# Kernel optimization log

Hardware: AMD Instinct MI355X
Metric: run time of the kernel (lower is better)

Reference implementation:

```python
import jax, jax.numpy as jnp
import numpy as np


def hilbert_perm(M: int) -> np.ndarray:
    """Permutation ordering the first M cells of a Hilbert curve on a 2^k x 2^k grid."""
    side = 1
    while side * side < M:
        side *= 2
    idx = np.arange(M)
    x = (idx % side).astype(np.int64)
    y = (idx // side).astype(np.int64)
    d = np.zeros(M, dtype=np.int64)
    s = side // 2
    while s > 0:
        rx = ((x & s) > 0).astype(np.int64)
        ry = ((y & s) > 0).astype(np.int64)
        d += s * s * ((3 * rx) ^ ry)
        swap = ry == 0
        flip = swap & (rx == 1)
        x2 = np.where(flip, s - 1 - x, x)
        y2 = np.where(flip, s - 1 - y, y)
        x, y = np.where(swap, y2, x2), np.where(swap, x2, y2)
        s //= 2
    return np.argsort(d, kind='stable')


SEGMENT_SIZE = 512


def setup_inputs() -> dict:
    key = jax.random.key(0)
    ks = jax.random.split(key, 5)
    B, M, H, D = 2, 8192, 8, 64
    hd = H * D  # 512
    q = jax.random.normal(ks[0], (B, M, H, D), dtype=jnp.float32)
    k = jax.random.normal(ks[1], (B, M, H, D), dtype=jnp.float32)
    v = jax.random.normal(ks[2], (B, M, H, D), dtype=jnp.float32)
    w_qkv = jax.random.normal(ks[3], (3 * hd, hd), dtype=jnp.float32) * (hd ** -0.5)
    w_out = jax.random.normal(ks[4], (hd, hd), dtype=jnp.float32) * (hd ** -0.5)
    return {"q": q, "k": k, "v": v, "w_qkv": w_qkv, "w_out": w_out}


def reference(q, k, v, w_qkv, w_out):
    B, M, H, D = q.shape
    hd = H * D
    S = SEGMENT_SIZE
    n_seg = M // S
    # Wrapper: mean over heads, then channel-repeat to hidden_dim
    x = q.mean(axis=2)                       # [B, M, D]
    x = jnp.tile(x, (1, 1, H))               # [B, M, hd]
    # HilbertAttentionCore: fused QKV projection
    qkv = jnp.einsum('bmc,fc->bmf', x, w_qkv)  # [B, M, 3*hd]
    qh, kh, vh = jnp.split(qkv, 3, axis=-1)
    # Hilbert-curve reordering (static permutation of seq dim)
    perm = jnp.asarray(hilbert_perm(M))
    inv = jnp.argsort(perm)
    def seg(t):
        t = t[:, perm]                       # reorder seq
        return t.reshape(B, n_seg, S, H, D)
    qs, ks_, vs = seg(qh), seg(kh), seg(vh)
    scale = D ** -0.5
    scores = jnp.einsum('bnshd,bnthd->bnhst', qs, ks_) * scale  # [B,n_seg,H,S,S]
    attn = jax.nn.softmax(scores, axis=-1)
    out = jnp.einsum('bnhst,bnthd->bnshd', attn, vs)            # [B,n_seg,S,H,D]
    out = out.reshape(B, M, hd)[:, inv]      # undo Hilbert ordering
    out = jnp.einsum('bmc,fc->bmf', out, w_out)  # output projection
    return out.reshape(B, M, H, D)
```

## Files before the change

kernel.cpp:

```cpp
#include <hip/hip_runtime.h>


typedef short bfrag __attribute__((ext_vector_type(8)));
typedef float ffrag __attribute__((ext_vector_type(4)));
typedef short svec4 __attribute__((ext_vector_type(4)));
typedef unsigned uvec4 __attribute__((ext_vector_type(4)));

__device__ inline short f2bf(float x) {
  unsigned u = __builtin_bit_cast(unsigned, x);
  u = (u + 0x7fffu + ((u >> 16) & 1u)) >> 16;
  return (short)u;
}
__device__ inline unsigned pk2f(float a, float b) {
  unsigned ua = (__builtin_bit_cast(unsigned, a) + 0x8000u) >> 16;
  unsigned ub = __builtin_bit_cast(unsigned, b) + 0x8000u;
  return ua | (ub & 0xffff0000u);
}
__device__ inline float fexp2(float x) {
#if __has_builtin(__builtin_amdgcn_exp2f)
  return __builtin_amdgcn_exp2f(x);
#else
  return __expf(x * 0.6931471805599453f);
#endif
}
__device__ inline void gload_lds16(const void* g, void* l) {
  __builtin_amdgcn_global_load_lds(
      (const __attribute__((address_space(1))) unsigned*)g,
      (__attribute__((address_space(3))) unsigned*)l, 16, 0, 0);
}

__device__ inline int d2xy128(int d) {
  int x = 0, y = 0, t = d;
  for (int s = 1; s < 128; s <<= 1) {
    int rx = 1 & (t >> 1);
    int ry = 1 & (t ^ rx);
    if (ry == 0) {
      if (rx == 1) { x = s - 1 - x; y = s - 1 - y; }
      int tt = x; x = y; y = tt;
    }
    x += s * rx;
    y += s * ry;
    t >>= 2;
  }
  return y * 128 + x;
}

__global__ __launch_bounds__(256) void prep_kernel(
    const float* __restrict__ q, const float* __restrict__ w_qkv,
    const float* __restrict__ w_out, short* __restrict__ xmean,
    short* __restrict__ weff, short* __restrict__ woutb,
    int* __restrict__ perm) {
  int i = blockIdx.x * 256 + threadIdx.x;
  if (i < 1048576) {
    int bm = i >> 6, d = i & 63;
    const float* p = q + (size_t)bm * 512 + d;
    float s = 0.f;
#pragma unroll
    for (int h = 0; h < 8; ++h) s += p[h * 64];
    xmean[i] = f2bf(s * 0.125f);
  } else if (i < 1048576 + 98304) {
    int j = i - 1048576;
    int f = j >> 6;
    const float* p = w_qkv + (size_t)f * 512 + (j & 63);
    float s = 0.f;
#pragma unroll
    for (int r = 0; r < 8; ++r) s += p[r * 64];
    if (f < 512) s *= 0.125f * 1.44269504088896f;
    weff[j] = f2bf(s);
  } else if (i < 1048576 + 98304 + 262144) {
    int j = i - 1048576 - 98304;
    woutb[j] = f2bf(w_out[j]);
  } else if (i < 1048576 + 98304 + 262144 + 8192) {
    int r = i - (1048576 + 98304 + 262144);
    perm[r] = d2xy128(r < 4096 ? r : r + 8192);
  }
}

__global__ __launch_bounds__(256) void qkv_kernel(
    const short* __restrict__ xmean, const short* __restrict__ weff,
    const int* __restrict__ perm, short* __restrict__ Qs,
    short* __restrict__ Ks, short* __restrict__ Vt) {
  int tid = threadIdx.x;
  int w = tid >> 6, lane = tid & 63;
  int ml = lane & 15, quad = lane >> 4;
  int rg = blockIdx.x >> 2, fq = blockIdx.x & 3;
  int r0 = rg * 64 + w * 16;
  int r = r0 + ml;
  int b = r >> 13, p = r & 8191;
  int src = (b << 13) + perm[p];
  bfrag a0 = *(const bfrag*)(xmean + (size_t)src * 64 + quad * 8);
  bfrag a1 = *(const bfrag*)(xmean + (size_t)src * 64 + 32 + quad * 8);
  int p0 = r0 & 8191;
  int bq = r0 >> 13;
  int nseg = p0 >> 9;
  int sbase = (p0 & 511) + quad * 4;

  auto loadW = [&](bfrag (&wf)[2], int nt) {
    const short* wp = weff + (size_t)(nt * 16 + ml) * 64 + quad * 8;
    wf[0] = *(const bfrag*)(wp);
    wf[1] = *(const bfrag*)(wp + 32);
  };
  auto emit = [&](bfrag (&wf)[2], int nt) {
    int f0 = nt * 16;
    ffrag acc = {0.f, 0.f, 0.f, 0.f};
    if (f0 < 1024) {
      acc = __builtin_amdgcn_mfma_f32_16x16x32_bf16(wf[0], a0, acc, 0, 0, 0);
      acc = __builtin_amdgcn_mfma_f32_16x16x32_bf16(wf[1], a1, acc, 0, 0, 0);
      short* dst = (f0 < 512) ? Qs : Ks;
      svec4 pk;
#pragma unroll
      for (int g = 0; g < 4; ++g) pk[g] = f2bf(acc[g]);
      *(svec4*)(dst + (size_t)(r0 + ml) * 512 + (f0 & 511) + quad * 4) = pk;
    } else {
      acc = __builtin_amdgcn_mfma_f32_16x16x32_bf16(a0, wf[0], acc, 0, 0, 0);
      acc = __builtin_amdgcn_mfma_f32_16x16x32_bf16(a1, wf[1], acc, 0, 0, 0);
      int fl = f0 + ml - 1024;
      int hh = fl >> 6, dd = fl & 63;
      svec4 pk;
#pragma unroll
      for (int g = 0; g < 4; ++g) pk[g] = f2bf(acc[g]);
      *(svec4*)(Vt + ((((size_t)bq * 16 + nseg) * 8 + hh) * 64 + dd) * 512 +
                sbase) = pk;
    }
  };

  int base = fq * 24;
  bfrag wA[2], wB[2];
  loadW(wA, base);
#pragma unroll 1
  for (int it = 0; it < 12; ++it) {
    int nt0 = base + it * 2;
    loadW(wB, nt0 + 1);
    emit(wA, nt0);
    loadW(wA, (it < 11) ? nt0 + 2 : base);
    emit(wB, nt0 + 1);
  }
}

__global__ __launch_bounds__(256, 2) void attn_kernel(
    const short* __restrict__ Qs, const short* __restrict__ Ks,
    const short* __restrict__ Vt, const int* __restrict__ perm,
    short* __restrict__ aout) {
  int tid = threadIdx.x;
  int w = tid >> 6, lane = tid & 63;
  int ml = lane & 15, quad = lane >> 4;
  int sh = blockIdx.x & 255;
  int qq = blockIdx.x >> 8;
  int b = sh >> 7;
  int n = (sh >> 3) & 15;
  int h = sh & 7;
  size_t segrow = (size_t)(b * 8192 + n * 512);
  const short* Qseg = Qs + segrow * 512 + h * 64;
  const short* Kseg = Ks + segrow * 512 + h * 64;
  const short* Vseg = Vt + (((size_t)(b * 16 + n) * 8 + h) * 64) * 512;
  int q0 = qq * 256 + w * 64;
  bfrag qa[4][2];
#pragma unroll
  for (int nq = 0; nq < 4; ++nq)
#pragma unroll
    for (int ks = 0; ks < 2; ++ks)
      qa[nq][ks] = *(const bfrag*)(Qseg + (size_t)(q0 + nq * 16 + ml) * 512 +
                                   ks * 32 + quad * 8);
  ffrag o[4][4];
  float lrun[4] = {0.f, 0.f, 0.f, 0.f};
#pragma unroll
  for (int nq = 0; nq < 4; ++nq)
#pragma unroll
    for (int dt = 0; dt < 4; ++dt) o[nq][dt] = (ffrag){0.f, 0.f, 0.f, 0.f};

  int lA = (((quad & 1) << 5) + ml) << 2;
  int lB = lA + 64;
  bool hi = quad >= 2;

  auto loadK = [&](bfrag (&kk)[2][2], int t0) {
#pragma unroll
    for (int mt = 0; mt < 2; ++mt)
#pragma unroll
      for (int ks = 0; ks < 2; ++ks)
        kk[mt][ks] = *(const bfrag*)(Kseg + (size_t)(t0 + mt * 16 + ml) * 512 +
                                     ks * 32 + quad * 8);
  };
  auto loadV = [&](bfrag (&vv)[4], int t0) {
#pragma unroll
    for (int dt = 0; dt < 4; ++dt)
      vv[dt] = *(const bfrag*)(Vseg + (size_t)(dt * 16 + ml) * 512 + t0 +
                               quad * 8);
  };
  auto body = [&](bfrag (&kk)[2][2], bfrag (&vv)[4]) {
#pragma unroll
    for (int nq = 0; nq < 4; ++nq) {
      ffrag c0 = {0.f, 0.f, 0.f, 0.f}, c1 = {0.f, 0.f, 0.f, 0.f};
      c0 = __builtin_amdgcn_mfma_f32_16x16x32_bf16(kk[0][0], qa[nq][0], c0, 0, 0, 0);
      c0 = __builtin_amdgcn_mfma_f32_16x16x32_bf16(kk[0][1], qa[nq][1], c0, 0, 0, 0);
      c1 = __builtin_amdgcn_mfma_f32_16x16x32_bf16(kk[1][0], qa[nq][0], c1, 0, 0, 0);
      c1 = __builtin_amdgcn_mfma_f32_16x16x32_bf16(kk[1][1], qa[nq][1], c1, 0, 0, 0);
      float e0 = fexp2(c0[0]), e1 = fexp2(c0[1]);
      float e2 = fexp2(c0[2]), e3 = fexp2(c0[3]);
      float e4 = fexp2(c1[0]), e5 = fexp2(c1[1]);
      float e6 = fexp2(c1[2]), e7 = fexp2(c1[3]);
      lrun[nq] += ((e0 + e1) + (e2 + e3)) + ((e4 + e5) + (e6 + e7));
      unsigned P0 = pk2f(e0, e1), P1 = pk2f(e2, e3);
      unsigned P2 = pk2f(e4, e5), P3 = pk2f(e6, e7);
      unsigned r0 = __builtin_amdgcn_ds_bpermute(lA, (int)P0);
      unsigned r1 = __builtin_amdgcn_ds_bpermute(lA, (int)P1);
      unsigned r2 = __builtin_amdgcn_ds_bpermute(lB, (int)P0);
      unsigned r3 = __builtin_amdgcn_ds_bpermute(lB, (int)P1);
      unsigned r4 = __builtin_amdgcn_ds_bpermute(lA, (int)P2);
      unsigned r5 = __builtin_amdgcn_ds_bpermute(lA, (int)P3);
      unsigned r6 = __builtin_amdgcn_ds_bpermute(lB, (int)P2);
      unsigned r7 = __builtin_amdgcn_ds_bpermute(lB, (int)P3);
      uvec4 pu;
      pu[0] = hi ? r4 : r0;
      pu[1] = hi ? r5 : r1;
      pu[2] = hi ? r6 : r2;
      pu[3] = hi ? r7 : r3;
      bfrag pa = __builtin_bit_cast(bfrag, pu);
#pragma unroll
      for (int dt = 0; dt < 4; ++dt)
        o[nq][dt] = __builtin_amdgcn_mfma_f32_16x16x32_bf16(vv[dt], pa,
                                                            o[nq][dt], 0, 0, 0);
    }
  };

  bfrag kA[2][2], kB[2][2], vA[4], vB[4];
  loadK(kA, 0);
  loadV(vA, 0);
#pragma unroll 1
  for (int jj = 0; jj < 8; ++jj) {
    int t1 = jj * 64 + 32;
    loadK(kB, t1);
    loadV(vB, t1);
    body(kA, vA);
    int t2 = (jj * 64 + 64) & 511;
    loadK(kA, t2);
    loadV(vA, t2);
    body(kB, vB);
  }
#pragma unroll
  for (int nq = 0; nq < 4; ++nq) {
    float l = lrun[nq];
    l += __shfl_xor(l, 16);
    l += __shfl_xor(l, 32);
    float inv = 1.f / l;
    int sout = q0 + nq * 16 + ml;
    int om = perm[n * 512 + sout];
    size_t base = ((size_t)(b * 8192 + om)) * 512 + h * 64;
#pragma unroll
    for (int dt = 0; dt < 4; ++dt) {
      svec4 pk;
#pragma unroll
      for (int g = 0; g < 4; ++g) pk[g] = f2bf(o[nq][dt][g] * inv);
      *(svec4*)(aout + base + dt * 16 + quad * 4) = pk;
    }
  }
}

__global__ __launch_bounds__(256, 2) void proj_kernel(
    const short* __restrict__ aout, const short* __restrict__ woutb,
    float* __restrict__ out) {
  __shared__ short As[2][128 * 64];
  __shared__ short Bs[2][128 * 64];
  int tid = threadIdx.x;
  int w = tid >> 6, lane = tid & 63;
  int ml = lane & 15, quad = lane >> 4;
  int rb = blockIdx.x & 127;
  int cb = blockIdx.x >> 7;
  int r0 = rb * 128, c0 = cb * 128;
  int wr = (w >> 1) * 64, wc = (w & 1) * 64;

  ffrag acc[4][4];
#pragma unroll
  for (int m = 0; m < 4; ++m)
#pragma unroll
    for (int n = 0; n < 4; ++n) acc[m][n] = (ffrag){0.f, 0.f, 0.f, 0.f};

  int srow = w * 32 + (lane >> 3);
  int scol = (lane & 7) * 8;
  const short* gA = aout + (size_t)(r0 + srow) * 512 + scol;
  const short* gB = woutb + (size_t)(c0 + srow) * 512 + scol;

  auto stage = [&](int buf, int k0) {
#pragma unroll
    for (int i = 0; i < 4; ++i) {
      gload_lds16(gA + (size_t)i * 8 * 512 + k0,
                  (char*)&As[buf][0] + w * 4096 + i * 1024);
      gload_lds16(gB + (size_t)i * 8 * 512 + k0,
                  (char*)&Bs[buf][0] + w * 4096 + i * 1024);
    }
  };
  auto compute = [&](int buf) {
#pragma unroll
    for (int kk = 0; kk < 2; ++kk) {
      bfrag af[4], bf[4];
#pragma unroll
      for (int m = 0; m < 4; ++m)
        af[m] = *(const bfrag*)&As[buf][(wr + m * 16 + ml) * 64 + kk * 32 +
                                        quad * 8];
#pragma unroll
      for (int n = 0; n < 4; ++n)
        bf[n] = *(const bfrag*)&Bs[buf][(wc + n * 16 + ml) * 64 + kk * 32 +
                                        quad * 8];
#pragma unroll
      for (int m = 0; m < 4; ++m)
#pragma unroll
        for (int n = 0; n < 4; ++n)
          acc[m][n] = __builtin_amdgcn_mfma_f32_16x16x32_bf16(bf[n], af[m],
                                                              acc[m][n], 0, 0, 0);
    }
  };

  stage(0, 0);
  __syncthreads();
  int cur = 0;
#pragma unroll 1
  for (int t = 0; t < 7; ++t) {
    stage(cur ^ 1, (t + 1) * 64);
    compute(cur);
    __syncthreads();
    cur ^= 1;
  }
  compute(cur);

#pragma unroll
  for (int m = 0; m < 4; ++m)
#pragma unroll
    for (int n = 0; n < 4; ++n)
      *(ffrag*)(out + (size_t)(r0 + wr + m * 16 + ml) * 512 + c0 + wc +
                n * 16 + quad * 4) = acc[m][n];
}

extern "C" void kernel_launch(void* const* d_in, const int* in_sizes, int n_in,
                              void* d_out, int out_size, void* d_ws,
                              size_t ws_size, hipStream_t stream) {
  const float* q = (const float*)d_in[0];
  const float* w_qkv = (const float*)d_in[3];
  const float* w_out = (const float*)d_in[4];
  float* out = (float*)d_out;

  char* ws = (char*)d_ws;
  int* perm = (int*)ws;
  short* xmean = (short*)(ws + 32768);
  short* weff = (short*)(ws + 2129920);
  short* woutb = (short*)(ws + 2326528);
  short* Qs = (short*)(ws + 2850816);
  short* Ks = (short*)(ws + 19628032);
  short* Vt = (short*)(ws + 36405248);
  short* aout = (short*)(ws + 53182464);

  prep_kernel<<<5536, 256, 0, stream>>>(q, w_qkv, w_out, xmean, weff, woutb,
                                        perm);
  qkv_kernel<<<1024, 256, 0, stream>>>(xmean, weff, perm, Qs, Ks, Vt);
  attn_kernel<<<512, 256, 0, stream>>>(Qs, Ks, Vt, perm, aout);
  proj_kernel<<<512, 256, 0, stream>>>(aout, woutb, out);
}
```

Baseline: 210.6 us.

## Stage shared K/V tiles through double-buffered swizzled LDS across waves

The four waves of a block previously each loaded the same K and V tiles straight from global memory into registers. They now cooperatively copy each 32-key K/V tile into a double-buffered LDS buffer, using direct global-to-LDS loads and XOR swizzling to avoid bank conflicts, then read MFMA fragments from LDS. The aim is to cut redundant global/L2 traffic by sharing each tile across waves. In exchange it adds a block-wide barrier per tile and the LDS reads, which limits how far the waves can drift out of step.

```diff
diff --git a/kernel.cpp b/kernel.cpp
--- a/kernel.cpp
+++ b/kernel.cpp
@@ -141,6 +141,8 @@
     const short* __restrict__ Qs, const short* __restrict__ Ks,
     const short* __restrict__ Vt, const int* __restrict__ perm,
     short* __restrict__ aout) {
+  __shared__ short Klds[2][32 * 64];
+  __shared__ short Vlds[2][64 * 32];
   int tid = threadIdx.x;
   int w = tid >> 6, lane = tid & 63;
   int ml = lane & 15, quad = lane >> 4;
@@ -172,21 +174,36 @@
   int lB = lA + 64;
   bool hi = quad >= 2;
 
-  auto loadK = [&](bfrag (&kk)[2][2], int t0) {
+  int krow = lane >> 3;
+  int kug = (lane & 7) ^ krow;
+  int vrow = w * 16 + (lane >> 2);
+  int vug = (lane & 3) ^ ((lane >> 3) & 3);
+
+  auto stage = [&](int buf, int t0) {
+    gload_lds16(Kseg + (size_t)(t0 + w * 8 + krow) * 512 + kug * 8,
+                (char*)&Klds[buf][0] + w * 1024);
+    gload_lds16(Vseg + (size_t)vrow * 512 + t0 + vug * 8,
+                (char*)&Vlds[buf][0] + w * 1024);
+  };
+
+  auto body = [&](int buf) {
+    const char* Kb = (const char*)&Klds[buf][0];
+    const char* Vb = (const char*)&Vlds[buf][0];
+    bfrag kk[2][2], vv[4];
 #pragma unroll
     for (int mt = 0; mt < 2; ++mt)
 #pragma unroll
-      for (int ks = 0; ks < 2; ++ks)
-        kk[mt][ks] = *(const bfrag*)(Kseg + (size_t)(t0 + mt * 16 + ml) * 512 +
-                                     ks * 32 + quad * 8);
-  };
-  auto loadV = [&](bfrag (&vv)[4], int t0) {
-#pragma unroll
-    for (int dt = 0; dt < 4; ++dt)
-      vv[dt] = *(const bfrag*)(Vseg + (size_t)(dt * 16 + ml) * 512 + t0 +
-                               quad * 8);
-  };
-  auto body = [&](bfrag (&kk)[2][2], bfrag (&vv)[4]) {
+      for (int ks = 0; ks < 2; ++ks) {
+        int row = mt * 16 + ml;
+        int byte = row * 128 + ks * 64 + quad * 16;
+        kk[mt][ks] = *(const bfrag*)(Kb + (byte ^ ((row & 7) << 4)));
+      }
+#pragma unroll
+    for (int dt = 0; dt < 4; ++dt) {
+      int row = dt * 16 + ml;
+      int byte = row * 64 + quad * 16;
+      vv[dt] = *(const bfrag*)(Vb + (byte ^ (((row >> 1) & 3) << 4)));
+    }
 #pragma unroll
     for (int nq = 0; nq < 4; ++nq) {
       ffrag c0 = {0.f, 0.f, 0.f, 0.f}, c1 = {0.f, 0.f, 0.f, 0.f};
@@ -222,20 +239,18 @@
     }
   };
 
-  bfrag kA[2][2], kB[2][2], vA[4], vB[4];
-  loadK(kA, 0);
-  loadV(vA, 0);
+  stage(0, 0);
+  __syncthreads();
+  int cur = 0;
 #pragma unroll 1
-  for (int jj = 0; jj < 8; ++jj) {
-    int t1 = jj * 64 + 32;
-    loadK(kB, t1);
-    loadV(vB, t1);
-    body(kA, vA);
-    int t2 = (jj * 64 + 64) & 511;
-    loadK(kA, t2);
-    loadV(vA, t2);
-    body(kB, vB);
-  }
+  for (int jj = 0; jj < 15; ++jj) {
+    stage(cur ^ 1, (jj + 1) * 32);
+    body(cur);
+    __syncthreads();
+    cur ^= 1;
+  }
+  body(cur);
+
 #pragma unroll
   for (int nq = 0; nq < 4; ++nq) {
     float l = lrun[nq];
```

Measured after the change: 203.9 us. 1.03x faster.
